# Kernel optimization log

Hardware: AMD Instinct MI355X
Metric: run time of the kernel (lower is better)

## Reference

```python
import jax, jax.numpy as jnp
import numpy as np
from jax import lax

HEADS = 4
DIM = 64
GATE_HID = 16


def setup_inputs() -> dict:
    key = jax.random.key(0)
    ks = jax.random.split(key, 12)
    b, c, h, w = 2, DIM, 48, 48
    s = 0.05
    x = jax.random.normal(ks[0], (b, c, h, w), jnp.float32)
    Wqkv = jax.random.normal(ks[1], (3 * c, c), jnp.float32) * s
    bqkv = jax.random.normal(ks[2], (3 * c,), jnp.float32) * s
    Wpos = jax.random.normal(ks[3], (3 * c, 1, 3, 3), jnp.float32) * s
    bpos = jax.random.normal(ks[4], (3 * c,), jnp.float32) * s
    Wg1 = jax.random.normal(ks[5], (GATE_HID, 1), jnp.float32) * 0.5
    bg1 = jax.random.normal(ks[6], (GATE_HID,), jnp.float32) * 0.1
    Wg2 = jax.random.normal(ks[7], (1, GATE_HID), jnp.float32) * 0.5
    bg2 = jax.random.normal(ks[8], (1,), jnp.float32) * 0.1
    Wproj = jax.random.normal(ks[9], (c, c), jnp.float32) * s
    bproj = jax.random.normal(ks[10], (c,), jnp.float32) * s
    return {"x": x, "Wqkv": Wqkv, "bqkv": bqkv, "Wpos": Wpos, "bpos": bpos,
            "Wg1": Wg1, "bg1": bg1, "Wg2": Wg2, "bg2": bg2,
            "Wproj": Wproj, "bproj": bproj}


def _forward(x, Wqkv, bqkv, Wpos, bpos, Wg1, bg1, Wg2, bg2, Wproj, bproj):
    b, c, h, w = x.shape
    n = h * w
    heads = HEADS
    hd = c // heads
    scale = hd ** -0.5
    # qkv 1x1 conv then 3x3 depthwise positional conv
    qkv = jnp.einsum('bchw,oc->bohw', x, Wqkv) + bqkv[None, :, None, None]
    qkv = lax.conv_general_dilated(
        qkv, Wpos, window_strides=(1, 1), padding='SAME',
        feature_group_count=3 * c,
        dimension_numbers=('NCHW', 'OIHW', 'NCHW')) + bpos[None, :, None, None]
    q, k, v = jnp.split(qkv, 3, axis=1)

    def to_heads(t):
        # [b,c,h,w] -> [b,heads,n,hd]
        return t.reshape(b, c, n).transpose(0, 2, 1).reshape(b, n, heads, hd).transpose(0, 2, 1, 3)

    q, k, v = to_heads(q), to_heads(k), to_heads(v)
    attn = jnp.einsum('bhid,bhjd->bhij', q, k) * scale  # [b,heads,n,n]
    prob = jax.nn.softmax(attn, axis=-1)
    entropy = -(prob * jnp.log(jnp.clip(prob, 1e-12))).sum(-1).mean(-1)  # [b,heads]
    # entropy gate: sigmoid(fc2(relu(fc1(e)))) * 0.9 + 0.1
    hgate = jax.nn.relu(entropy[..., None] @ Wg1.T + bg1)  # [b,heads,16]
    ratio = jax.nn.sigmoid(hgate @ Wg2.T + bg2)[..., 0] * 0.9 + 0.1  # [b,heads]
    # dynamic per-(batch,head) top-k along rows via rank threshold
    keep = jnp.clip(jnp.ceil(ratio * n).astype(jnp.int32), 1, n)  # [b,heads]
    sorted_desc = -jnp.sort(-attn, axis=-1)  # [b,heads,n,n]
    idx = jnp.broadcast_to((keep - 1)[:, :, None, None], (b, heads, n, 1))
    thresh = jnp.take_along_axis(sorted_desc, idx, axis=-1)  # [b,heads,n,1]
    sparse = jnp.where(attn >= thresh, attn, -jnp.inf)
    p = jax.nn.softmax(sparse, axis=-1)
    out = jnp.einsum('bhij,bhjd->bhid', p, v)  # [b,heads,n,hd]
    out = out.transpose(0, 2, 1, 3).reshape(b, n, c)
    out = out @ Wproj.T + bproj
    return out.transpose(0, 2, 1).reshape(b, c, h, w)


def reference(x, Wqkv, bqkv, Wpos, bpos, Wg1, bg1, Wg2, bg2, Wproj, bproj):
    return _forward(x, Wqkv, bqkv, Wpos, bpos, Wg1, bg1, Wg2, bg2, Wproj, bproj)
```

## Files before the change

### kernel.cpp

```cpp
#include <hip/hip_runtime.h>
#include <hip/hip_fp16.h>


typedef _Float16 half8_t __attribute__((ext_vector_type(8)));
typedef float floatx4 __attribute__((ext_vector_type(4)));

union HU { unsigned short s; _Float16 h; };
__device__ __forceinline__ _Float16 ubits_h(unsigned short u) {
  HU c; c.s = u; return c.h;
}
__device__ __forceinline__ _Float16 key_h(unsigned k) {
  unsigned short u = (k & 0x8000u) ? (unsigned short)(k & 0x7FFFu)
                                   : (unsigned short)((~k) & 0xFFFFu);
  return ubits_h(u);
}

__device__ __forceinline__ uint2 hist_select_p(const unsigned* h, int lane,
                                               unsigned keepN) {
  uint2 w = ((const uint2*)h)[lane];
  unsigned c0 = w.x & 0xFFFFu, c1 = w.x >> 16;
  unsigned c2 = w.y & 0xFFFFu, c3 = w.y >> 16;
  unsigned inc = c0 + c1 + c2 + c3;
#pragma unroll
  for (int off = 1; off < 64; off <<= 1) {
    unsigned t = __shfl_up(inc, off);
    if (lane >= off) inc += t;
  }
  unsigned total = __shfl(inc, 63);
  unsigned above = total - inc;
  unsigned a3 = above;
  unsigned a2 = a3 + c3;
  unsigned a1 = a2 + c2;
  unsigned a0 = a1 + c1;
  bool has = false;
  unsigned B_l = 0, A_l = 0;
  if (a3 < keepN && a3 + c3 >= keepN) { has = true; B_l = lane * 4 + 3; A_l = a3; }
  else if (a2 < keepN && a2 + c2 >= keepN) { has = true; B_l = lane * 4 + 2; A_l = a2; }
  else if (a1 < keepN && a1 + c1 >= keepN) { has = true; B_l = lane * 4 + 1; A_l = a1; }
  else if (a0 < keepN && a0 + c0 >= keepN) { has = true; B_l = lane * 4 + 0; A_l = a0; }
  unsigned long long m = __ballot(has);
  int src = __ffsll(m) - 1;
  return make_uint2(__shfl(B_l, src), __shfl(A_l, src));
}

__global__ __launch_bounds__(256) void k_qkv(const float* __restrict__ x,
                                             const float* __restrict__ W,
                                             const float* __restrict__ bias,
                                             float* __restrict__ out,
                                             float* __restrict__ ent) {
  if (blockIdx.x == 0 && threadIdx.x < 8) ent[threadIdx.x] = 0.f;
  int blk = blockIdx.x;
  int chunk = blk % 9;
  int og = (blk / 9) % 48;
  int b = blk / (9 * 48);
  int o0 = og * 4;
  int pos = chunk * 256 + threadIdx.x;
  const float* xb = x + b * 64 * 2304 + pos;
  const float* w0 = W + (o0 + 0) * 64;
  const float* w1 = W + (o0 + 1) * 64;
  const float* w2 = W + (o0 + 2) * 64;
  const float* w3 = W + (o0 + 3) * 64;
  float a0 = bias[o0 + 0], a1 = bias[o0 + 1];
  float a2 = bias[o0 + 2], a3 = bias[o0 + 3];
#pragma unroll
  for (int c = 0; c < 64; c++) {
    float xv = xb[c * 2304];
    a0 = fmaf(w0[c], xv, a0);
    a1 = fmaf(w1[c], xv, a1);
    a2 = fmaf(w2[c], xv, a2);
    a3 = fmaf(w3[c], xv, a3);
  }
  out[(b * 192 + o0 + 0) * 2304 + pos] = a0;
  out[(b * 192 + o0 + 1) * 2304 + pos] = a1;
  out[(b * 192 + o0 + 2) * 2304 + pos] = a2;
  out[(b * 192 + o0 + 3) * 2304 + pos] = a3;
}

__global__ __launch_bounds__(256) void k_dw(const float* __restrict__ qkv,
                                            const float* __restrict__ Wpos,
                                            const float* __restrict__ bpos,
                                            _Float16* __restrict__ q2,
                                            _Float16* __restrict__ k2,
                                            _Float16* __restrict__ vt) {
  __shared__ float smem[8][384];
  int blk = blockIdx.x;
  int chunk = blk % 9;
  int half = (blk / 9) % 2;
  int sel = (blk / 18) % 3;
  int head = (blk / 54) % 4;
  int b = blk / 216;
  int chbase = sel * 64 + head * 16 + half * 8;
  int bh = b * 4 + head;
  int tid = threadIdx.x;
  int p0 = chunk * 256;
  int baserow = p0 / 48;
  int rA = min(max(baserow - 1, 0), 40);

  const float* src = qkv + (size_t)(b * 192 + chbase) * 2304;
#pragma unroll
  for (int l = 0; l < 12; l++) {
    int idx = tid + l * 256;
    int ch = idx / 384;
    int off = idx - ch * 384;
    int rr = off / 48;
    int cc = off - rr * 48;
    smem[ch][off] = src[(size_t)ch * 2304 + (rA + rr) * 48 + cc];
  }
  __syncthreads();

  int pos = p0 + tid;
  int yy = pos / 48, xx = pos - yy * 48;
  int ry = yy - rA;
  float accv[8];
#pragma unroll
  for (int d = 0; d < 8; d++) {
    const float* w = Wpos + (chbase + d) * 9;
    float a = bpos[chbase + d];
#pragma unroll
    for (int dy = -1; dy <= 1; dy++) {
      int y2 = yy + dy;
      if ((unsigned)y2 < 48u) {
#pragma unroll
        for (int dx = -1; dx <= 1; dx++) {
          int x2 = xx + dx;
          if ((unsigned)x2 < 48u)
            a = fmaf(w[(dy + 1) * 3 + (dx + 1)], smem[d][(ry + dy) * 48 + x2],
                     a);
        }
      }
    }
    accv[d] = a;
  }

  if (sel == 2) {
#pragma unroll
    for (int d = 0; d < 8; d++)
      vt[((size_t)bh * 16 + half * 8 + d) * 2304 + pos] = (_Float16)accv[d];
  } else {
    _Float16 h1[8], h2[8];
#pragma unroll
    for (int d = 0; d < 8; d++) {
      float a = (sel == 0) ? accv[d] * 0.25f : accv[d];
      h1[d] = (_Float16)a;
      h2[d] = (_Float16)(a - (float)h1[d]);
    }
    _Float16* dst = ((sel == 0) ? q2 : k2) + ((size_t)bh * 2304 + pos) * 32;
    *(uint4*)(dst + half * 8) = *(uint4*)&h1[0];
    *(uint4*)(dst + 16 + half * 8) = *(uint4*)&h2[0];
  }
}

template <bool STORE>
__global__ __launch_bounds__(256) void k_ent_t(const _Float16* __restrict__ q2,
                                               const _Float16* __restrict__ k2,
                                               float* __restrict__ ent,
                                               _Float16* __restrict__ lgH) {
  __shared__ __align__(16) _Float16 tBuf[4][16][72];
  __shared__ float sWv[4][16], uWv[4][16];

  int blk = blockIdx.x;
  int rowtile = blk % 144;
  int bh = blk / 144;
  int row0 = rowtile * 16;
  int tid = threadIdx.x, lane = tid & 63, wave = tid >> 6;
  int m16 = lane & 15, quad = lane >> 4;

  const half8_t* q2v =
      (const half8_t*)(q2 + ((size_t)bh * 2304 + row0 + m16) * 32);
  half8_t A1 = q2v[quad];
  half8_t zh = {};
  half8_t A2 = (lane < 32) ? A1 : zh;
  const half8_t* kbase = (const half8_t*)(k2 + (size_t)bh * 2304 * 32);

  float s[4] = {0.f, 0.f, 0.f, 0.f}, u[4] = {0.f, 0.f, 0.f, 0.f};
  for (int g = 0; g < 9; g++) {
#pragma unroll
    for (int tt = 0; tt < 4; tt++) {
      int t = g * 4 + tt;
      int col = wave * 576 + t * 16 + m16;
      const half8_t* kk = kbase + (size_t)col * 4;
      half8_t b1 = kk[quad & 1];
      half8_t b2 = kk[2 + (quad & 1)];
      floatx4 acc = {};
      acc = __builtin_amdgcn_mfma_f32_16x16x32_f16(A2, b2, acc, 0, 0, 0);
      acc = __builtin_amdgcn_mfma_f32_16x16x32_f16(A1, b1, acc, 0, 0, 0);
#pragma unroll
      for (int i = 0; i < 4; i++) {
        if (STORE) tBuf[wave][quad * 4 + i][tt * 16 + m16] = (_Float16)acc[i];
        float e = __expf(acc[i]);
        s[i] += e;
        u[i] = fmaf(acc[i], e, u[i]);
      }
    }
    if (STORE) {
      __syncthreads();
      int rb = lane >> 3, seg = lane & 7;
#pragma unroll
      for (int it = 0; it < 2; it++) {
        int rr = it * 8 + rb;
        uint4 vv = *(const uint4*)&tBuf[wave][rr][seg * 8];
        *(uint4*)(lgH + ((size_t)bh * 2304 + row0 + rr) * 2304 + wave * 576 +
                  g * 64 + seg * 8) = vv;
      }
      __syncthreads();
    }
  }
#pragma unroll
  for (int off = 1; off < 16; off <<= 1) {
#pragma unroll
    for (int i = 0; i < 4; i++) {
      s[i] += __shfl_xor(s[i], off);
      u[i] += __shfl_xor(u[i], off);
    }
  }
  if (m16 == 0) {
#pragma unroll
    for (int i = 0; i < 4; i++) {
      sWv[wave][quad * 4 + i] = s[i];
      uWv[wave][quad * 4 + i] = u[i];
    }
  }
  __syncthreads();
  if (tid < 16) {
    float S = sWv[0][tid] + sWv[1][tid] + sWv[2][tid] + sWv[3][tid];
    float U = uWv[0][tid] + uWv[1][tid] + uWv[2][tid] + uWv[3][tid];
    float er = __logf(S) - U / S;
    er += __shfl_xor(er, 1);
    er += __shfl_xor(er, 2);
    er += __shfl_xor(er, 4);
    er += __shfl_xor(er, 8);
    if (tid == 0) atomicAdd(&ent[bh], er);
  }
}

__global__ __launch_bounds__(512, 6) void k_attn_f(
    const _Float16* __restrict__ q2, const _Float16* __restrict__ k2,
    const _Float16* __restrict__ vt, const float* __restrict__ ent,
    const float* __restrict__ Wg1, const float* __restrict__ bg1,
    const float* __restrict__ Wg2, const float* __restrict__ bg2,
    float* __restrict__ oh) {
  __shared__ __align__(16) _Float16 lg[8 * 2320];
  __shared__ unsigned hist[8][128];
  __shared__ float sS[8];
  __shared__ __align__(16) float redSh[8][64];

  int blk = blockIdx.x;
  int bh = blk & 7;
  int tile = blk >> 3;
  int row0 = tile * 8;
  int tid = threadIdx.x, lane = tid & 63, wave = tid >> 6;
  int m16 = lane & 15, quad = lane >> 4;

  float eAvg = ent[bh] * (1.f / 2304.f);
  float gacc = bg2[0];
#pragma unroll
  for (int i = 0; i < 16; i++) {
    float h = fmaxf(fmaf(eAvg, Wg1[i], bg1[i]), 0.f);
    gacc = fmaf(h, Wg2[i], gacc);
  }
  float ratio = 0.9f / (1.f + __expf(-gacc)) + 0.1f;
  int kp = (int)ceilf(ratio * 2304.f);
  unsigned keep = (unsigned)min(max(kp, 1), 2304);

  {
    const half8_t* q2v =
        (const half8_t*)(q2 + ((size_t)bh * 2304 + row0 + (m16 & 7)) * 32);
    half8_t A1 = q2v[quad];
    half8_t zh = {};
    half8_t A2 = (lane < 32) ? A1 : zh;
    const half8_t* kbase = (const half8_t*)(k2 + (size_t)bh * 2304 * 32);
#pragma unroll 2
    for (int t = 0; t < 18; t++) {
      int col = wave * 288 + t * 16 + m16;
      const half8_t* kk = kbase + (size_t)col * 4;
      half8_t b1 = kk[quad & 1];
      half8_t b2 = kk[2 + (quad & 1)];
      floatx4 acc = {};
      acc = __builtin_amdgcn_mfma_f32_16x16x32_f16(A2, b2, acc, 0, 0, 0);
      acc = __builtin_amdgcn_mfma_f32_16x16x32_f16(A1, b1, acc, 0, 0, 0);
      if (quad < 2) {
#pragma unroll
        for (int i = 0; i < 4; i++)
          lg[(quad * 4 + i) * 2320 + col] = (_Float16)acc[i];
      }
    }
  }
  __syncthreads();

  {
    char* rb = (char*)lg + wave * 4640;
    const uint4* s4 = (const uint4*)rb;
    uint4 q0 = s4[lane];
    uint4 q1 = s4[lane + 64];
    uint4 q2r = s4[lane + 128];
    uint4 q3 = s4[lane + 192];
    uint2 q4 = *(const uint2*)(rb + 4096 + lane * 8);
    unsigned wb[18] = {q0.x, q0.y, q0.z, q0.w, q1.x, q1.y, q1.z, q1.w,
                       q2r.x, q2r.y, q2r.z, q2r.w, q3.x, q3.y, q3.z, q3.w,
                       q4.x, q4.y};
    unsigned kb[18];
#pragma unroll
    for (int i = 0; i < 18; i++)
      kb[i] = wb[i] ^ (((wb[i] >> 15) & 0x00010001u) * 0x7FFFu + 0x80008000u);

    unsigned* h = hist[wave];
    h[lane] = 0u;
    h[lane + 64] = 0u;
#pragma unroll
    for (int i = 0; i < 18; i++) {
      unsigned b1 = (kb[i] >> 8) & 0xFFu;
      unsigned b2 = kb[i] >> 24;
      atomicAdd(&h[b1 >> 1], 1u << ((b1 & 1) << 4));
      atomicAdd(&h[b2 >> 1], 1u << ((b2 & 1) << 4));
    }
    uint2 s1 = hist_select_p(h, lane, keep);
    unsigned B = s1.x;
    unsigned keep2 = keep - s1.y;

    h[lane] = 0u;
    h[lane + 64] = 0u;
#pragma unroll
    for (int i = 0; i < 18; i++) {
      unsigned klo = kb[i] & 0xFFFFu;
      unsigned khi = kb[i] >> 16;
      if ((klo >> 8) == B) {
        unsigned lb = klo & 0xFFu;
        atomicAdd(&h[lb >> 1], 1u << ((lb & 1) << 4));
      }
      if ((khi >> 8) == B) {
        unsigned lb = khi & 0xFFu;
        atomicAdd(&h[lb >> 1], 1u << ((lb & 1) << 4));
      }
    }
    uint2 s2 = hist_select_p(h, lane, keep2);
    _Float16 th_h = key_h((B << 8) | s2.x);

    float sp = 0.f;
    uint4* prow4 = (uint4*)rb;
#pragma unroll
    for (int g = 0; g < 4; g++) {
      uint4 o;
      unsigned ow[4];
#pragma unroll
      for (int wj = 0; wj < 4; wj++) {
        unsigned w = wb[g * 4 + wj];
        _Float16 hlo = ubits_h((unsigned short)(w & 0xFFFFu));
        _Float16 hhi = ubits_h((unsigned short)(w >> 16));
        float plo = (hlo >= th_h) ? __expf((float)hlo) : 0.f;
        float phi = (hhi >= th_h) ? __expf((float)hhi) : 0.f;
        __half2 hp = __floats2half2_rn(plo, phi);
        ow[wj] = *(unsigned*)&hp;
        if (wj == 0) sp += ((plo + phi));
      }
      o.x = ow[0]; o.y = ow[1]; o.z = ow[2]; o.w = ow[3];
      prow4[lane + g * 64] = o;
      {
        _Float16 h2a = ubits_h((unsigned short)(wb[g * 4 + 1] & 0xFFFFu));
        _Float16 h2b = ubits_h((unsigned short)(wb[g * 4 + 1] >> 16));
        _Float16 h3a = ubits_h((unsigned short)(wb[g * 4 + 2] & 0xFFFFu));
        _Float16 h3b = ubits_h((unsigned short)(wb[g * 4 + 2] >> 16));
        _Float16 h4a = ubits_h((unsigned short)(wb[g * 4 + 3] & 0xFFFFu));
        _Float16 h4b = ubits_h((unsigned short)(wb[g * 4 + 3] >> 16));
        float p2 = (h2a >= th_h) ? __expf((float)h2a) : 0.f;
        float p3 = (h2b >= th_h) ? __expf((float)h2b) : 0.f;
        float p4 = (h3a >= th_h) ? __expf((float)h3a) : 0.f;
        float p5 = (h3b >= th_h) ? __expf((float)h3b) : 0.f;
        float p6 = (h4a >= th_h) ? __expf((float)h4a) : 0.f;
        float p7 = (h4b >= th_h) ? __expf((float)h4b) : 0.f;
        sp += (p2 + p3);
        sp += (p4 + p5) + (p6 + p7);
      }
    }
    {
      _Float16 h0 = ubits_h((unsigned short)(wb[16] & 0xFFFFu));
      _Float16 h1 = ubits_h((unsigned short)(wb[16] >> 16));
      _Float16 h2 = ubits_h((unsigned short)(wb[17] & 0xFFFFu));
      _Float16 h3 = ubits_h((unsigned short)(wb[17] >> 16));
      float p0 = (h0 >= th_h) ? __expf((float)h0) : 0.f;
      float p1 = (h1 >= th_h) ? __expf((float)h1) : 0.f;
      float p2 = (h2 >= th_h) ? __expf((float)h2) : 0.f;
      float p3 = (h3 >= th_h) ? __expf((float)h3) : 0.f;
      sp += (p0 + p1) + (p2 + p3);
      uint2 o;
      __half2 hp0 = __floats2half2_rn(p0, p1); o.x = *(unsigned*)&hp0;
      __half2 hp1 = __floats2half2_rn(p2, p3); o.y = *(unsigned*)&hp1;
      *(uint2*)(rb + 4096 + lane * 8) = o;
    }
#pragma unroll
    for (int off = 1; off < 64; off <<= 1) sp += __shfl_xor(sp, off);
    if (lane == 0) sS[wave] = sp;
  }
  __syncthreads();

  {
    int g = wave >> 2;
    int jq = wave & 3;
    const _Float16* vrow = vt + ((size_t)bh * 16 + m16) * 2304;
    const _Float16* prow = lg + (size_t)(g * 4 + (m16 & 3)) * 2320;
    int jb0 = jq * 576 + quad * 8;
    floatx4 acc = {};
#pragma unroll 6
    for (int t = 0; t < 18; t++) {
      int jb = jb0 + t * 32;
      half8_t a2 = *(const half8_t*)&prow[jb];
      half8_t b2 = *(const half8_t*)&vrow[jb];
      acc = __builtin_amdgcn_mfma_f32_16x16x32_f16(a2, b2, acc, 0, 0, 0);
    }
    if (lane < 16) {
      *(floatx4*)&redSh[wave][m16 * 4] = acc;
    }
  }
  __syncthreads();
  if (tid < 128) {
    int g = tid >> 6, idx = tid & 63;
    int r = idx & 3, d = idx >> 2;
    float s2 = redSh[g * 4 + 0][d * 4 + r] + redSh[g * 4 + 1][d * 4 + r] +
               redSh[g * 4 + 2][d * 4 + r] + redSh[g * 4 + 3][d * 4 + r];
    oh[((size_t)(bh * 2304 + row0 + g * 4 + r)) * 16 + d] =
        s2 / sS[g * 4 + r];
  }
}

__global__ __launch_bounds__(256) void k_proj(const float* __restrict__ oh,
                                              const float* __restrict__ Wp,
                                              const float* __restrict__ bp,
                                              float* __restrict__ out) {
  int blk = blockIdx.x;
  int chunk = blk % 9;
  int cog = (blk / 9) % 16;
  int b = blk / (9 * 16);
  int co0 = cog * 4;
  int pos = chunk * 256 + threadIdx.x;
  float a0 = bp[co0 + 0], a1 = bp[co0 + 1], a2 = bp[co0 + 2], a3 = bp[co0 + 3];
#pragma unroll
  for (int head = 0; head < 4; head++) {
    const float4* op =
        (const float4*)(oh + ((size_t)((b * 4 + head) * 2304 + pos)) * 16);
#pragma unroll
    for (int p = 0; p < 4; p++) {
      float4 o4 = op[p];
#pragma unroll
      for (int i = 0; i < 4; i++) {
        const float* wr = Wp + (co0 + i) * 64 + head * 16 + p * 4;
        float* ai = (i == 0) ? &a0 : ((i == 1) ? &a1 : ((i == 2) ? &a2 : &a3));
        *ai = fmaf(wr[0], o4.x, *ai);
        *ai = fmaf(wr[1], o4.y, *ai);
        *ai = fmaf(wr[2], o4.z, *ai);
        *ai = fmaf(wr[3], o4.w, *ai);
      }
    }
  }
  out[(b * 64 + co0 + 0) * 2304 + pos] = a0;
  out[(b * 64 + co0 + 1) * 2304 + pos] = a1;
  out[(b * 64 + co0 + 2) * 2304 + pos] = a2;
  out[(b * 64 + co0 + 3) * 2304 + pos] = a3;
}

extern "C" void kernel_launch(void* const* d_in, const int* in_sizes, int n_in,
                              void* d_out, int out_size, void* d_ws,
                              size_t ws_size, hipStream_t stream) {
  const float* x    = (const float*)d_in[0];
  const float* Wqkv = (const float*)d_in[1];
  const float* bqkv = (const float*)d_in[2];
  const float* Wpos = (const float*)d_in[3];
  const float* bpos = (const float*)d_in[4];
  const float* Wg1  = (const float*)d_in[5];
  const float* bg1  = (const float*)d_in[6];
  const float* Wg2  = (const float*)d_in[7];
  const float* bg2  = (const float*)d_in[8];
  const float* Wpr  = (const float*)d_in[9];
  const float* bpr  = (const float*)d_in[10];
  float* out = (float*)d_out;

  char* base = (char*)d_ws;
  float* qkv_raw = (float*)base;
  float* oh = qkv_raw + 884736;
  float* ent = oh + 294912;
  _Float16* q2 = (_Float16*)(ent + 8);
  _Float16* k2 = q2 + 589824;
  _Float16* vt = k2 + 589824;

  hipLaunchKernelGGL(k_qkv, dim3(2 * 48 * 9), dim3(256), 0, stream,
                     x, Wqkv, bqkv, qkv_raw, ent);
  hipLaunchKernelGGL(k_dw, dim3(432), dim3(256), 0, stream,
                     qkv_raw, Wpos, bpos, q2, k2, vt);
  hipLaunchKernelGGL((k_ent_t<false>), dim3(8 * 144), dim3(256), 0, stream,
                     q2, k2, ent, (_Float16*)nullptr);
  hipLaunchKernelGGL(k_attn_f, dim3(2304), dim3(512), 0, stream,
                     q2, k2, vt, ent, Wg1, bg1, Wg2, bg2, oh);
  hipLaunchKernelGGL(k_proj, dim3(2 * 16 * 9), dim3(256), 0, stream,
                     oh, Wpr, bpr, out);
}
```

Baseline: 229.4 us.

## Replace LDS histogram radix select with ballot-based bitwise threshold search

The per-row top-k threshold search drops the two-pass shared-memory histogram, which relied on packed LDS atomics and prefix scans. It now runs a 16-step bitwise binary search over the sortable fp16 keys held in registers. Each step counts the keys at or above a candidate across the wave with ballot and popcount, and stops early once the count equals keep exactly. This removes contended LDS atomics and the histogram buffer, at the cost of up to 16×36 compare/ballot operations per wave and more live registers for the 36 unpacked keys.

```diff
diff --git a/kernel.cpp b/kernel.cpp
--- a/kernel.cpp
+++ b/kernel.cpp
@@ -13,34 +13,6 @@
   unsigned short u = (k & 0x8000u) ? (unsigned short)(k & 0x7FFFu)
                                    : (unsigned short)((~k) & 0xFFFFu);
   return ubits_h(u);
-}
-
-__device__ __forceinline__ uint2 hist_select_p(const unsigned* h, int lane,
-                                               unsigned keepN) {
-  uint2 w = ((const uint2*)h)[lane];
-  unsigned c0 = w.x & 0xFFFFu, c1 = w.x >> 16;
-  unsigned c2 = w.y & 0xFFFFu, c3 = w.y >> 16;
-  unsigned inc = c0 + c1 + c2 + c3;
-#pragma unroll
-  for (int off = 1; off < 64; off <<= 1) {
-    unsigned t = __shfl_up(inc, off);
-    if (lane >= off) inc += t;
-  }
-  unsigned total = __shfl(inc, 63);
-  unsigned above = total - inc;
-  unsigned a3 = above;
-  unsigned a2 = a3 + c3;
-  unsigned a1 = a2 + c2;
-  unsigned a0 = a1 + c1;
-  bool has = false;
-  unsigned B_l = 0, A_l = 0;
-  if (a3 < keepN && a3 + c3 >= keepN) { has = true; B_l = lane * 4 + 3; A_l = a3; }
-  else if (a2 < keepN && a2 + c2 >= keepN) { has = true; B_l = lane * 4 + 2; A_l = a2; }
-  else if (a1 < keepN && a1 + c1 >= keepN) { has = true; B_l = lane * 4 + 1; A_l = a1; }
-  else if (a0 < keepN && a0 + c0 >= keepN) { has = true; B_l = lane * 4 + 0; A_l = a0; }
-  unsigned long long m = __ballot(has);
-  int src = __ffsll(m) - 1;
-  return make_uint2(__shfl(B_l, src), __shfl(A_l, src));
 }
 
 __global__ __launch_bounds__(256) void k_qkv(const float* __restrict__ x,
@@ -240,7 +212,6 @@
     const float* __restrict__ Wg2, const float* __restrict__ bg2,
     float* __restrict__ oh) {
   __shared__ __align__(16) _Float16 lg[8 * 2320];
-  __shared__ unsigned hist[8][128];
   __shared__ float sS[8];
   __shared__ __align__(16) float redSh[8][64];
 
@@ -298,42 +269,28 @@
     unsigned wb[18] = {q0.x, q0.y, q0.z, q0.w, q1.x, q1.y, q1.z, q1.w,
                        q2r.x, q2r.y, q2r.z, q2r.w, q3.x, q3.y, q3.z, q3.w,
                        q4.x, q4.y};
-    unsigned kb[18];
-#pragma unroll
-    for (int i = 0; i < 18; i++)
-      kb[i] = wb[i] ^ (((wb[i] >> 15) & 0x00010001u) * 0x7FFFu + 0x80008000u);
-
-    unsigned* h = hist[wave];
-    h[lane] = 0u;
-    h[lane + 64] = 0u;
+    unsigned ku[36];
 #pragma unroll
     for (int i = 0; i < 18; i++) {
-      unsigned b1 = (kb[i] >> 8) & 0xFFu;
-      unsigned b2 = kb[i] >> 24;
-      atomicAdd(&h[b1 >> 1], 1u << ((b1 & 1) << 4));
-      atomicAdd(&h[b2 >> 1], 1u << ((b2 & 1) << 4));
-    }
-    uint2 s1 = hist_select_p(h, lane, keep);
-    unsigned B = s1.x;
-    unsigned keep2 = keep - s1.y;
-
-    h[lane] = 0u;
-    h[lane + 64] = 0u;
-#pragma unroll
-    for (int i = 0; i < 18; i++) {
-      unsigned klo = kb[i] & 0xFFFFu;
-      unsigned khi = kb[i] >> 16;
-      if ((klo >> 8) == B) {
-        unsigned lb = klo & 0xFFu;
-        atomicAdd(&h[lb >> 1], 1u << ((lb & 1) << 4));
-      }
-      if ((khi >> 8) == B) {
-        unsigned lb = khi & 0xFFu;
-        atomicAdd(&h[lb >> 1], 1u << ((lb & 1) << 4));
-      }
-    }
-    uint2 s2 = hist_select_p(h, lane, keep2);
-    _Float16 th_h = key_h((B << 8) | s2.x);
+      unsigned kbi =
+          wb[i] ^ (((wb[i] >> 15) & 0x00010001u) * 0x7FFFu + 0x80008000u);
+      ku[2 * i + 0] = kbi & 0xFFFFu;
+      ku[2 * i + 1] = kbi >> 16;
+    }
+
+    unsigned T = 0u;
+    for (int bit = 15; bit >= 0; --bit) {
+      unsigned cand = T | (1u << bit);
+      unsigned cnt = 0u;
+#pragma unroll
+      for (int i = 0; i < 36; i++)
+        cnt += (unsigned)__popcll(__ballot(ku[i] >= cand));
+      if (cnt >= keep) {
+        T = cand;
+        if (cnt == keep) break;
+      }
+    }
+    _Float16 th_h = key_h(T);
 
     float sp = 0.f;
     uint4* prow4 = (uint4*)rb;
```

After: 228.4 us. No clear change (-0.4%).
